# Kernel tuning notes

Measured on AMD Instinct MI355X. Metric: run time of the kernel, lower is better.

The kernel has to match this reference:

```python
import jax, jax.numpy as jnp
import numpy as np

N_IND, N_COM, N_TRU = 100000, 100000, 100000
N = N_IND + N_COM + N_TRU
E = 4800000
H = 64
NUM_CLASSES = 2


def _sage(x, src, dst, Wl, Wr, b):
    # PyG SAGEConv (mean aggr): out = lin_l(mean_{j in N(i)} x_j) + lin_r(x_i)
    msg = x[src]                                   # [E, H] gather
    agg = jax.ops.segment_sum(msg, dst, num_segments=N)           # [N, H]
    cnt = jax.ops.segment_sum(jnp.ones((src.shape[0],), x.dtype), dst, num_segments=N)
    mean = agg / jnp.maximum(cnt, 1.0)[:, None]
    return mean @ Wl + x @ Wr + b


def setup_inputs() -> dict:
    key = jax.random.key(0)
    ks = jax.random.split(key, 20)
    inp = {
        "x_individual": jax.random.normal(ks[0], (N_IND, 32), jnp.float32),
        "x_company": jax.random.normal(ks[1], (N_COM, 48), jnp.float32),
        "x_trust": jax.random.normal(ks[2], (N_TRU, 24), jnp.float32),
        "edge_index": jax.random.randint(ks[3], (2, E), 0, N, jnp.int64 if jax.config.jax_enable_x64 else jnp.int32),
    }
    def lin(k, fan_in, fan_out):
        s = 1.0 / np.sqrt(fan_in)
        return jax.random.uniform(k, (fan_in, fan_out), jnp.float32, -s, s)
    inp.update({
        "W_ind": lin(ks[4], 32, H), "b_ind": jnp.zeros((H,), jnp.float32),
        "W_com": lin(ks[5], 48, H), "b_com": jnp.zeros((H,), jnp.float32),
        "W_tru": lin(ks[6], 24, H), "b_tru": jnp.zeros((H,), jnp.float32),
        "W1l": lin(ks[7], H, H), "W1r": lin(ks[8], H, H), "b1": jnp.zeros((H,), jnp.float32),
        "W2l": lin(ks[9], H, H), "W2r": lin(ks[10], H, H), "b2": jnp.zeros((H,), jnp.float32),
        "Wc1": lin(ks[11], H, H // 2), "bc1": jnp.zeros((H // 2,), jnp.float32),
        "Wc2": lin(ks[12], H // 2, NUM_CLASSES), "bc2": jnp.zeros((NUM_CLASSES,), jnp.float32),
    })
    return inp


def reference(x_individual, x_company, x_trust, edge_index,
              W_ind, b_ind, W_com, b_com, W_tru, b_tru,
              W1l, W1r, b1, W2l, W2r, b2, Wc1, bc1, Wc2, bc2):
    # per-type linear encoders, then concat along node dim
    x = jnp.concatenate([
        x_individual @ W_ind + b_ind,
        x_company @ W_com + b_com,
        x_trust @ W_tru + b_tru,
    ], axis=0)  # [N, H]
    src, dst = edge_index[0], edge_index[1]
    x = jax.nn.relu(_sage(x, src, dst, W1l, W1r, b1))
    x = jax.nn.relu(_sage(x, src, dst, W2l, W2r, b2))
    # classifier MLP (dropout is identity in eval mode)
    h = jax.nn.relu(x @ Wc1 + bc1)
    return h @ Wc2 + bc2  # [N, num_classes]
```

## Files before the change

kernel.cpp:

```cpp
#include <hip/hip_runtime.h>

#define N_IND 100000
#define N_COM 100000
#define N_TRU 100000
#define NTOT  300000
#define NEDGE 4800000
#define HDIM  64
#define CHUNK 8192
#define NCHUNKS 586
#define NCB 293
#define CAP 18432
#define PADW 33
#define NTILES32 9375

typedef float v4f __attribute__((ext_vector_type(4)));
typedef unsigned short v4u __attribute__((ext_vector_type(4)));
typedef unsigned short v8u __attribute__((ext_vector_type(8)));
typedef _Float16 v8h __attribute__((ext_vector_type(8)));

static __device__ __forceinline__ float elem4(const float4 v, int j) {
  return j == 0 ? v.x : j == 1 ? v.y : j == 2 ? v.z : v.w;
}

static __device__ __forceinline__ unsigned short f2h(float f) {
  _Float16 h = (_Float16)f;
  return __builtin_bit_cast(unsigned short, h);
}
static __device__ __forceinline__ float h2f(unsigned short u) {
  return (float)__builtin_bit_cast(_Float16, u);
}

static __device__ __forceinline__ void fmix2(float& alo, float& ahi, unsigned pk) {
  asm("v_fma_mix_f32 %0, %1, 1.0, %0 op_sel:[0,0,0] op_sel_hi:[1,0,0]"
      : "+v"(alo) : "v"(pk));
  asm("v_fma_mix_f32 %0, %1, 1.0, %0 op_sel:[1,0,0] op_sel_hi:[1,0,0]"
      : "+v"(ahi) : "v"(pk));
}

static __device__ __forceinline__ void store_rows_f16(
    unsigned short* __restrict__ out, float* __restrict__ st, const float* acc,
    int node0, int rows, int tid, bool active) {
#pragma unroll
  for (int stage = 0; stage < 2; ++stage) {
    __syncthreads();
    if (active) {
#pragma unroll
      for (int j = 0; j < 32; ++j) st[tid * PADW + j] = acc[stage * 32 + j];
    }
    __syncthreads();
#pragma unroll
    for (int it = 0; it < 8; ++it) {
      int e = it * 256 + tid;
      int r = e >> 3;
      int c = (e & 7) * 4;
      if (r < rows) {
        v4u o;
        o.x = f2h(st[r * PADW + c + 0]);
        o.y = f2h(st[r * PADW + c + 1]);
        o.z = f2h(st[r * PADW + c + 2]);
        o.w = f2h(st[r * PADW + c + 3]);
        *(v4u*)(out + (size_t)(node0 + r) * HDIM + stage * 32 + c) = o;
      }
    }
  }
}

template <int K>
__global__ __launch_bounds__(256, 2) void encode_kernel(
    const float* __restrict__ xin, const float* __restrict__ W,
    const float* __restrict__ b, unsigned short* __restrict__ xhout, int n, int base) {
  __shared__ float st[256 * PADW];
  int tid = threadIdx.x;
  int node0 = blockIdx.x * 256;
  int node = node0 + tid;
  bool active = node < n;
  int rows = min(256, n - node0);
  float acc[HDIM];
  if (active) {
    float4 row[K / 4];
    const float4* xv = (const float4*)(xin + (size_t)node * K);
#pragma unroll
    for (int i = 0; i < K / 4; ++i) row[i] = xv[i];
#pragma unroll
    for (int f = 0; f < HDIM; ++f) acc[f] = b[f];
#pragma unroll
    for (int k4 = 0; k4 < K / 4; ++k4) {
#pragma unroll
      for (int j = 0; j < 4; ++j) {
        float xs = elem4(row[k4], j);
        int k = k4 * 4 + j;
#pragma unroll
        for (int f = 0; f < HDIM; ++f) acc[f] += xs * W[k * HDIM + f];
      }
    }
  }
  store_rows_f16(xhout + (size_t)base * HDIM, st, acc, node0, rows, tid, active);
}

__global__ __launch_bounds__(256) void prep_weights_kernel(
    const float* __restrict__ W1l, const float* __restrict__ W1r,
    const float* __restrict__ W2l, const float* __restrict__ W2r,
    unsigned short* __restrict__ out, int* __restrict__ ccur) {
  const float* Ws[4] = {W1l, W1r, W2l, W2r};
  int tid = threadIdx.x;
  for (int b = tid; b < NCB; b += 256) ccur[b] = b * CAP;
  for (int m = 0; m < 4; ++m) {
    const float* W = Ws[m];
    unsigned short* o = out + m * 4096;
    for (int idx = tid; idx < 4096; idx += 256) {
      int j = idx & 7;
      int l = (idx >> 3) & 63;
      int ts = idx >> 9;
      int t = ts >> 1, s = ts & 1;
      int k = s * 32 + (l >> 4) * 8 + j;
      int n = t * 16 + (l & 15);
      o[idx] = f2h(W[k * HDIM + n]);
    }
  }
}

__global__ __launch_bounds__(512) void coarse_scatter_kernel(
    const int* __restrict__ src, const int* __restrict__ dst,
    int* __restrict__ ccur, unsigned* __restrict__ packed, int e) {
  __shared__ int h[NCB];
  __shared__ int gofs[NCB];
  __shared__ int sv[512];
  __shared__ unsigned vals[CHUNK];
  __shared__ unsigned short bid[CHUNK];
  int tid = threadIdx.x;
  int start = blockIdx.x * CHUNK;
  int len = min(CHUNK, e - start);

  for (int i = tid; i < NCB; i += 512) h[i] = 0;
  __syncthreads();

  int dreg[CHUNK / 512];
#pragma unroll
  for (int k = 0; k < CHUNK / 512; ++k) {
    int i = k * 512 + tid;
    dreg[k] = (i < len) ? dst[start + i] : -1;
    if (i < len) atomicAdd(&h[dreg[k] >> 10], 1);
  }
  __syncthreads();

  sv[tid] = (tid < NCB) ? h[tid] : 0;
  __syncthreads();
  for (int o = 1; o < 512; o <<= 1) {
    int y = (tid >= o) ? sv[tid - o] : 0;
    __syncthreads();
    sv[tid] += y;
    __syncthreads();
  }
  if (tid < NCB) {
    int c = h[tid];
    int lo = (tid == 0) ? 0 : sv[tid - 1];
    int gb = (c > 0) ? atomicAdd(&ccur[tid], c) : 0;
    gofs[tid] = gb - lo;
    h[tid] = lo;
  }
  __syncthreads();

#pragma unroll
  for (int k = 0; k < CHUNK / 512; ++k) {
    int i = k * 512 + tid;
    if (i < len) {
      int d = dreg[k];
      int s = src[start + i];
      int b = d >> 10;
      int slot = atomicAdd(&h[b], 1);
      vals[slot] = ((unsigned)s << 10) | (unsigned)(d & 1023);
      bid[slot] = (unsigned short)b;
    }
  }
  __syncthreads();

  for (int i = tid; i < len; i += 512) {
    int b = bid[i];
    packed[gofs[b] + i] = vals[i];
  }
}

__global__ __launch_bounds__(1024) void sort_coarse_kernel(
    const unsigned* __restrict__ packed, const int* __restrict__ ccur,
    int* __restrict__ eidx, int* __restrict__ nodeoff, int* __restrict__ deg) {
  __shared__ int cnts[1024];
  __shared__ int cur[1024];
  __shared__ int sv[1024];
  int cb = blockIdx.x;
  int tid = threadIdx.x;
  cnts[tid] = 0;
  __syncthreads();
  int base = cb * CAP;
  int cnt = ccur[cb] - base;
  for (int i = tid; i < cnt; i += 1024)
    atomicAdd(&cnts[packed[base + i] & 1023u], 1);
  __syncthreads();
  int c = cnts[tid];
  sv[tid] = c;
  __syncthreads();
  for (int o = 1; o < 1024; o <<= 1) {
    int y = (tid >= o) ? sv[tid - o] : 0;
    __syncthreads();
    sv[tid] += y;
    __syncthreads();
  }
  int ex = sv[tid] - c;
  cur[tid] = ex;
  int node = (cb << 10) + tid;
  if (node < NTOT) { deg[node] = c; nodeoff[node] = base + ex; }
  __syncthreads();
  for (int i = tid; i < cnt; i += 1024) {
    unsigned pr = packed[base + i];
    int dl = (int)(pr & 1023u);
    int r = atomicAdd(&cur[dl], 1);
    eidx[base + r] = (int)(pr >> 10);
  }
}

#define SMPAD 72
template <bool LAYER2>
__global__ __launch_bounds__(256, 6) void agg_combine_kernel(
    const unsigned short* __restrict__ xh, const int* __restrict__ off,
    const int* __restrict__ deg, const int* __restrict__ eidx,
    const unsigned short* __restrict__ wfrag,
    const float* __restrict__ bb,
    unsigned short* __restrict__ outh,
    const float* __restrict__ Wc1, const float* __restrict__ bc1,
    const float* __restrict__ Wc2, const float* __restrict__ bc2,
    float* __restrict__ dout) {
  __shared__ unsigned short smean[32 * SMPAD];
  __shared__ float st[32 * 68 + 8];
  __shared__ float sW1[LAYER2 ? 2048 : 8];
  int tid = threadIdx.x;
  int node0 = blockIdx.x * 32;

  {
    int nit = tid >> 3;
    int lane8 = tid & 7;
    int node = node0 + nit;
    int start = off[node];
    int d = deg[node];
    const char* xb = (const char*)xh;
    unsigned rofs = (unsigned)(lane8 << 4);
    float acc[16];
#pragma unroll
    for (int j = 0; j < 16; ++j) acc[j] = 0.f;
    int i = 0;
    for (; i + 8 <= d; i += 8) {
      const int* ep = eidx + start + i;
      int s[8];
#pragma unroll
      for (int k = 0; k < 8; ++k) s[k] = ep[k];
      uint4 v[8];
#pragma unroll
      for (int k = 0; k < 8; ++k)
        v[k] = *(const uint4*)(xb + ((((unsigned)s[k]) << 7) + rofs));
#pragma unroll
      for (int k = 0; k < 8; ++k) {
        float* a = &acc[(k & 1) * 8];
        fmix2(a[0], a[1], v[k].x);
        fmix2(a[2], a[3], v[k].y);
        fmix2(a[4], a[5], v[k].z);
        fmix2(a[6], a[7], v[k].w);
      }
    }
    if (i + 4 <= d) {
      const int* ep = eidx + start + i;
      int s[4];
#pragma unroll
      for (int k = 0; k < 4; ++k) s[k] = ep[k];
      uint4 v[4];
#pragma unroll
      for (int k = 0; k < 4; ++k)
        v[k] = *(const uint4*)(xb + ((((unsigned)s[k]) << 7) + rofs));
#pragma unroll
      for (int k = 0; k < 4; ++k) {
        float* a = &acc[(k & 1) * 8];
        fmix2(a[0], a[1], v[k].x);
        fmix2(a[2], a[3], v[k].y);
        fmix2(a[4], a[5], v[k].z);
        fmix2(a[6], a[7], v[k].w);
      }
      i += 4;
    }
    for (; i < d; ++i) {
      int s = eidx[start + i];
      uint4 v = *(const uint4*)(xb + ((((unsigned)s) << 7) + rofs));
      fmix2(acc[0], acc[1], v.x);
      fmix2(acc[2], acc[3], v.y);
      fmix2(acc[4], acc[5], v.z);
      fmix2(acc[6], acc[7], v.w);
    }
    float inv = 1.0f / (float)(d > 0 ? d : 1);
    v8u o;
#pragma unroll
    for (int j = 0; j < 8; ++j) o[j] = f2h((acc[j] + acc[8 + j]) * inv);
    *(v8u*)&smean[nit * SMPAD + lane8 * 8] = o;
  }
  if (LAYER2) {
    for (int i = tid; i < 2048; i += 256) sW1[i] = Wc1[i];
  }
  __syncthreads();

  int wid = tid >> 6;
  int lane = tid & 63;
  int mlo = lane & 15;
  int quad = lane >> 4;
  {
    const v8h* wf = (const v8h*)wfrag;
#pragma unroll
    for (int p = 0; p < 2; ++p) {
      int task = wid * 2 + p;
      int rt = task >> 2, cb = task & 3;
      v8h BL0 = wf[(cb * 2 + 0) * 64 + lane];
      v8h BL1 = wf[(cb * 2 + 1) * 64 + lane];
      v8h BR0 = wf[512 + (cb * 2 + 0) * 64 + lane];
      v8h BR1 = wf[512 + (cb * 2 + 1) * 64 + lane];
      float bias = bb[cb * 16 + mlo];
      int arow = rt * 16 + mlo;
      v8h Am0 = *(const v8h*)&smean[arow * SMPAD + quad * 8];
      v8h Am1 = *(const v8h*)&smean[arow * SMPAD + quad * 8 + 32];
      const _Float16* xrow =
          (const _Float16*)xh + (size_t)(node0 + arow) * HDIM + quad * 8;
      v8h Ax0 = *(const v8h*)(xrow);
      v8h Ax1 = *(const v8h*)(xrow + 32);
      v4f acc = {bias, bias, bias, bias};
      acc = __builtin_amdgcn_mfma_f32_16x16x32_f16(Am0, BL0, acc, 0, 0, 0);
      acc = __builtin_amdgcn_mfma_f32_16x16x32_f16(Am1, BL1, acc, 0, 0, 0);
      acc = __builtin_amdgcn_mfma_f32_16x16x32_f16(Ax0, BR0, acc, 0, 0, 0);
      acc = __builtin_amdgcn_mfma_f32_16x16x32_f16(Ax1, BR1, acc, 0, 0, 0);
#pragma unroll
      for (int r = 0; r < 4; ++r)
        st[(rt * 16 + quad * 4 + r) * 68 + cb * 16 + mlo] = fmaxf(acc[r], 0.f);
    }
  }
  __syncthreads();

  if (!LAYER2) {
    int r = tid >> 3;
    int c = (tid & 7) * 8;
    const float* ap = &st[r * 68 + c];
    v8u o;
#pragma unroll
    for (int j = 0; j < 8; ++j) o[j] = f2h(ap[j]);
    *(v8u*)(outh + (size_t)(node0 + r) * HDIM + c) = o;
  } else {
    int nd = tid >> 3;
    int f = (tid & 7) * 4;
    float h0 = bc1[f], h1 = bc1[f + 1], h2 = bc1[f + 2], h3 = bc1[f + 3];
    const float* xr = &st[nd * 68];
#pragma unroll
    for (int k = 0; k < 64; ++k) {
      float xv = xr[k];
      h0 += xv * sW1[k * 32 + f + 0];
      h1 += xv * sW1[k * 32 + f + 1];
      h2 += xv * sW1[k * 32 + f + 2];
      h3 += xv * sW1[k * 32 + f + 3];
    }
    h0 = fmaxf(h0, 0.f); h1 = fmaxf(h1, 0.f);
    h2 = fmaxf(h2, 0.f); h3 = fmaxf(h3, 0.f);
    float o0 = h0 * Wc2[f * 2 + 0] + h1 * Wc2[(f + 1) * 2 + 0] +
               h2 * Wc2[(f + 2) * 2 + 0] + h3 * Wc2[(f + 3) * 2 + 0];
    float o1 = h0 * Wc2[f * 2 + 1] + h1 * Wc2[(f + 1) * 2 + 1] +
               h2 * Wc2[(f + 2) * 2 + 1] + h3 * Wc2[(f + 3) * 2 + 1];
#pragma unroll
    for (int m = 4; m >= 1; m >>= 1) {
      o0 += __shfl_xor(o0, m);
      o1 += __shfl_xor(o1, m);
    }
    if ((tid & 7) == 0) {
      float2 ov;
      ov.x = o0 + bc2[0];
      ov.y = o1 + bc2[1];
      *(float2*)(dout + (size_t)(node0 + nd) * 2) = ov;
    }
  }
}

extern "C" void kernel_launch(void* const* d_in, const int* in_sizes, int n_in,
                              void* d_out, int out_size, void* d_ws, size_t ws_size,
                              hipStream_t stream) {
  const float* x_ind = (const float*)d_in[0];
  const float* x_com = (const float*)d_in[1];
  const float* x_tru = (const float*)d_in[2];
  const int*   ei    = (const int*)d_in[3];
  const float* W_ind = (const float*)d_in[4];
  const float* b_ind = (const float*)d_in[5];
  const float* W_com = (const float*)d_in[6];
  const float* b_com = (const float*)d_in[7];
  const float* W_tru = (const float*)d_in[8];
  const float* b_tru = (const float*)d_in[9];
  const float* W1l = (const float*)d_in[10];
  const float* W1r = (const float*)d_in[11];
  const float* b1  = (const float*)d_in[12];
  const float* W2l = (const float*)d_in[13];
  const float* W2r = (const float*)d_in[14];
  const float* b2  = (const float*)d_in[15];
  const float* Wc1 = (const float*)d_in[16];
  const float* bc1 = (const float*)d_in[17];
  const float* Wc2 = (const float*)d_in[18];
  const float* bc2 = (const float*)d_in[19];

  const int* srcp = ei;
  const int* dstp = ei + NEDGE;

  size_t fcount = (size_t)NTOT * HDIM;
  size_t pksz = (size_t)NCB * CAP;
  unsigned* packed = (unsigned*)d_ws;
  unsigned short* xh0 = (unsigned short*)(packed + pksz);
  unsigned short* xh1 = xh0 + fcount;
  int* eidx    = (int*)(xh1 + fcount);
  int* nodeoff = eidx + pksz;
  int* deg     = nodeoff + NTOT;
  int* ccur    = deg + NTOT;
  unsigned short* wfrag = (unsigned short*)((((size_t)(ccur + NCB)) + 15) & ~(size_t)15);
  size_t needed = (size_t)((char*)(wfrag + 4 * 4096) - (char*)d_ws) + 64;
  if (ws_size < needed) return;

  prep_weights_kernel<<<1, 256, 0, stream>>>(W1l, W1r, W2l, W2r, wfrag, ccur);

  encode_kernel<32><<<(N_IND + 255) / 256, 256, 0, stream>>>(x_ind, W_ind, b_ind, xh0, N_IND, 0);
  encode_kernel<48><<<(N_COM + 255) / 256, 256, 0, stream>>>(x_com, W_com, b_com, xh0, N_COM, N_IND);
  encode_kernel<24><<<(N_TRU + 255) / 256, 256, 0, stream>>>(x_tru, W_tru, b_tru, xh0, N_TRU, N_IND + N_COM);

  coarse_scatter_kernel<<<NCHUNKS, 512, 0, stream>>>(srcp, dstp, ccur, packed, NEDGE);
  sort_coarse_kernel<<<NCB, 1024, 0, stream>>>(packed, ccur, eidx, nodeoff, deg);

  agg_combine_kernel<false><<<NTILES32, 256, 0, stream>>>(
      xh0, nodeoff, deg, eidx, wfrag, b1, xh1, nullptr, nullptr, nullptr, nullptr, nullptr);

  agg_combine_kernel<true><<<NTILES32, 256, 0, stream>>>(
      xh1, nodeoff, deg, eidx, wfrag + 2 * 4096, b2, nullptr, Wc1, bc1, Wc2, bc2,
      (float*)d_out);
}
```

Baseline: 493.4 us.

## Fuse encoders and edge scatter into one front kernel; parallelize weight prep

Merges the three per-type encoder launches and the coarse edge-scatter launch into a single kernel that dispatches on block index. Independent encode and scatter work can then run concurrently and three launch gaps disappear. The scatter is reworked for 256-thread blocks with 32 destinations per thread, the weight-prep kernel is spread over 65 blocks instead of one, and the aggregation kernel's occupancy hint is raised from 6 to 7. Risks: shared memory is sized for the larger scatter path and the launch bound allows two blocks per CU, which may limit encode occupancy; the scatter blocks also use more registers.

```diff
diff --git a/kernel.cpp b/kernel.cpp
--- a/kernel.cpp
+++ b/kernel.cpp
@@ -12,6 +12,9 @@
 #define CAP 18432
 #define PADW 33
 #define NTILES32 9375
+#define NBLK_ENC1 391
+#define NBLK_ENC  1173
+#define NBLK_MEGA 1759
 
 typedef float v4f __attribute__((ext_vector_type(4)));
 typedef unsigned short v4u __attribute__((ext_vector_type(4)));
@@ -66,12 +69,12 @@
 }
 
 template <int K>
-__global__ __launch_bounds__(256, 2) void encode_kernel(
+static __device__ void encode_body(
     const float* __restrict__ xin, const float* __restrict__ W,
-    const float* __restrict__ b, unsigned short* __restrict__ xhout, int n, int base) {
-  __shared__ float st[256 * PADW];
+    const float* __restrict__ b, unsigned short* __restrict__ xhout,
+    int n, int base, int blk, float* st) {
   int tid = threadIdx.x;
-  int node0 = blockIdx.x * 256;
+  int node0 = blk * 256;
   int node = node0 + tid;
   bool active = node < n;
   int rows = min(256, n - node0);
@@ -97,87 +100,113 @@
   store_rows_f16(xhout + (size_t)base * HDIM, st, acc, node0, rows, tid, active);
 }
 
-__global__ __launch_bounds__(256) void prep_weights_kernel(
-    const float* __restrict__ W1l, const float* __restrict__ W1r,
-    const float* __restrict__ W2l, const float* __restrict__ W2r,
-    unsigned short* __restrict__ out, int* __restrict__ ccur) {
-  const float* Ws[4] = {W1l, W1r, W2l, W2r};
+static __device__ void scatter_body(
+    const int* __restrict__ src, const int* __restrict__ dst,
+    int* __restrict__ ccur, unsigned* __restrict__ packed, int e, int blk,
+    char* smem) {
+  int* h = (int*)smem;
+  int* gofs = h + NCB;
+  int* sv = gofs + NCB;
+  unsigned* vals = (unsigned*)(sv + 512);
+  unsigned short* sbid = (unsigned short*)(vals + CHUNK);
   int tid = threadIdx.x;
-  for (int b = tid; b < NCB; b += 256) ccur[b] = b * CAP;
-  for (int m = 0; m < 4; ++m) {
-    const float* W = Ws[m];
-    unsigned short* o = out + m * 4096;
-    for (int idx = tid; idx < 4096; idx += 256) {
-      int j = idx & 7;
-      int l = (idx >> 3) & 63;
-      int ts = idx >> 9;
-      int t = ts >> 1, s = ts & 1;
-      int k = s * 32 + (l >> 4) * 8 + j;
-      int n = t * 16 + (l & 15);
-      o[idx] = f2h(W[k * HDIM + n]);
-    }
-  }
-}
-
-__global__ __launch_bounds__(512) void coarse_scatter_kernel(
-    const int* __restrict__ src, const int* __restrict__ dst,
-    int* __restrict__ ccur, unsigned* __restrict__ packed, int e) {
-  __shared__ int h[NCB];
-  __shared__ int gofs[NCB];
-  __shared__ int sv[512];
-  __shared__ unsigned vals[CHUNK];
-  __shared__ unsigned short bid[CHUNK];
-  int tid = threadIdx.x;
-  int start = blockIdx.x * CHUNK;
+  int start = blk * CHUNK;
   int len = min(CHUNK, e - start);
 
-  for (int i = tid; i < NCB; i += 512) h[i] = 0;
-  __syncthreads();
-
-  int dreg[CHUNK / 512];
-#pragma unroll
-  for (int k = 0; k < CHUNK / 512; ++k) {
-    int i = k * 512 + tid;
+  for (int i = tid; i < NCB; i += 256) h[i] = 0;
+  __syncthreads();
+
+  int dreg[CHUNK / 256];
+#pragma unroll
+  for (int k = 0; k < CHUNK / 256; ++k) {
+    int i = k * 256 + tid;
     dreg[k] = (i < len) ? dst[start + i] : -1;
     if (i < len) atomicAdd(&h[dreg[k] >> 10], 1);
   }
   __syncthreads();
 
   sv[tid] = (tid < NCB) ? h[tid] : 0;
+  sv[tid + 256] = (tid + 256 < NCB) ? h[tid + 256] : 0;
   __syncthreads();
   for (int o = 1; o < 512; o <<= 1) {
-    int y = (tid >= o) ? sv[tid - o] : 0;
-    __syncthreads();
-    sv[tid] += y;
-    __syncthreads();
-  }
-  if (tid < NCB) {
-    int c = h[tid];
-    int lo = (tid == 0) ? 0 : sv[tid - 1];
-    int gb = (c > 0) ? atomicAdd(&ccur[tid], c) : 0;
-    gofs[tid] = gb - lo;
-    h[tid] = lo;
-  }
-  __syncthreads();
-
-#pragma unroll
-  for (int k = 0; k < CHUNK / 512; ++k) {
-    int i = k * 512 + tid;
+    int y0 = (tid >= o) ? sv[tid - o] : 0;
+    int y1 = sv[tid + 256 - o];
+    __syncthreads();
+    sv[tid] += y0;
+    sv[tid + 256] += y1;
+    __syncthreads();
+  }
+  for (int b = tid; b < NCB; b += 256) {
+    int c = h[b];
+    int lo = (b == 0) ? 0 : sv[b - 1];
+    int gb = (c > 0) ? atomicAdd(&ccur[b], c) : 0;
+    gofs[b] = gb - lo;
+    h[b] = lo;
+  }
+  __syncthreads();
+
+#pragma unroll
+  for (int k = 0; k < CHUNK / 256; ++k) {
+    int i = k * 256 + tid;
     if (i < len) {
       int d = dreg[k];
       int s = src[start + i];
       int b = d >> 10;
       int slot = atomicAdd(&h[b], 1);
       vals[slot] = ((unsigned)s << 10) | (unsigned)(d & 1023);
-      bid[slot] = (unsigned short)b;
-    }
-  }
-  __syncthreads();
-
-  for (int i = tid; i < len; i += 512) {
-    int b = bid[i];
+      sbid[slot] = (unsigned short)b;
+    }
+  }
+  __syncthreads();
+
+  for (int i = tid; i < len; i += 256) {
+    int b = sbid[i];
     packed[gofs[b] + i] = vals[i];
   }
+}
+
+__global__ __launch_bounds__(256, 2) void mega_front_kernel(
+    const float* __restrict__ x_ind, const float* __restrict__ W_ind, const float* __restrict__ b_ind,
+    const float* __restrict__ x_com, const float* __restrict__ W_com, const float* __restrict__ b_com,
+    const float* __restrict__ x_tru, const float* __restrict__ W_tru, const float* __restrict__ b_tru,
+    unsigned short* __restrict__ xh0,
+    const int* __restrict__ src, const int* __restrict__ dst,
+    int* __restrict__ ccur, unsigned* __restrict__ packed) {
+  __shared__ __align__(16) char smem[53568];
+  int bid = blockIdx.x;
+  if (bid < NBLK_ENC1) {
+    encode_body<32>(x_ind, W_ind, b_ind, xh0, N_IND, 0, bid, (float*)smem);
+  } else if (bid < 2 * NBLK_ENC1) {
+    encode_body<48>(x_com, W_com, b_com, xh0, N_COM, N_IND, bid - NBLK_ENC1, (float*)smem);
+  } else if (bid < NBLK_ENC) {
+    encode_body<24>(x_tru, W_tru, b_tru, xh0, N_TRU, N_IND + N_COM, bid - 2 * NBLK_ENC1,
+                    (float*)smem);
+  } else {
+    scatter_body(src, dst, ccur, packed, NEDGE, bid - NBLK_ENC, smem);
+  }
+}
+
+__global__ __launch_bounds__(256) void prep_weights_kernel(
+    const float* __restrict__ W1l, const float* __restrict__ W1r,
+    const float* __restrict__ W2l, const float* __restrict__ W2r,
+    unsigned short* __restrict__ out, int* __restrict__ ccur) {
+  int bid = blockIdx.x;
+  int tid = threadIdx.x;
+  if (bid == 64) {
+    for (int b = tid; b < NCB; b += 256) ccur[b] = b * CAP;
+    return;
+  }
+  int idx = bid * 256 + tid;
+  int m = idx >> 12;
+  int id2 = idx & 4095;
+  const float* W = (m == 0) ? W1l : (m == 1) ? W1r : (m == 2) ? W2l : W2r;
+  int j = id2 & 7;
+  int l = (id2 >> 3) & 63;
+  int ts = id2 >> 9;
+  int t = ts >> 1, s = ts & 1;
+  int k = s * 32 + (l >> 4) * 8 + j;
+  int n = t * 16 + (l & 15);
+  out[m * 4096 + id2] = f2h(W[k * HDIM + n]);
 }
 
 __global__ __launch_bounds__(1024) void sort_coarse_kernel(
@@ -219,7 +248,7 @@
 
 #define SMPAD 72
 template <bool LAYER2>
-__global__ __launch_bounds__(256, 6) void agg_combine_kernel(
+__global__ __launch_bounds__(256, 7) void agg_combine_kernel(
     const unsigned short* __restrict__ xh, const int* __restrict__ off,
     const int* __restrict__ deg, const int* __restrict__ eidx,
     const unsigned short* __restrict__ wfrag,
@@ -417,13 +446,12 @@
   size_t needed = (size_t)((char*)(wfrag + 4 * 4096) - (char*)d_ws) + 64;
   if (ws_size < needed) return;
 
-  prep_weights_kernel<<<1, 256, 0, stream>>>(W1l, W1r, W2l, W2r, wfrag, ccur);
-
-  encode_kernel<32><<<(N_IND + 255) / 256, 256, 0, stream>>>(x_ind, W_ind, b_ind, xh0, N_IND, 0);
-  encode_kernel<48><<<(N_COM + 255) / 256, 256, 0, stream>>>(x_com, W_com, b_com, xh0, N_COM, N_IND);
-  encode_kernel<24><<<(N_TRU + 255) / 256, 256, 0, stream>>>(x_tru, W_tru, b_tru, xh0, N_TRU, N_IND + N_COM);
-
-  coarse_scatter_kernel<<<NCHUNKS, 512, 0, stream>>>(srcp, dstp, ccur, packed, NEDGE);
+  prep_weights_kernel<<<65, 256, 0, stream>>>(W1l, W1r, W2l, W2r, wfrag, ccur);
+
+  mega_front_kernel<<<NBLK_MEGA, 256, 0, stream>>>(
+      x_ind, W_ind, b_ind, x_com, W_com, b_com, x_tru, W_tru, b_tru,
+      xh0, srcp, dstp, ccur, packed);
+
   sort_coarse_kernel<<<NCB, 1024, 0, stream>>>(packed, ccur, eidx, nodeoff, deg);
 
   agg_combine_kernel<false><<<NTILES32, 256, 0, stream>>>(
```

New measurement: 463.8 us. 1.06x faster.
